# Kernel optimization log

Hardware: AMD Instinct MI355X
Metric: run time of the kernel (lower is better)

## Reference

```python
import jax, jax.numpy as jnp
from jax import lax
import numpy as np

B, C, H, W = 4, 1024, 64, 64
HEAD_DIM = 8
HEADS = C // HEAD_DIM  # 128
EPS = 1e-15
BN_EPS = 1e-5
DN = ('NCHW', 'OIHW', 'NCHW')


def setup_inputs() -> dict:
    key = jax.random.key(0)
    ks = jax.random.split(key, 8)
    s = lambda k, shp, scale: jax.random.normal(k, shp, jnp.float32) * scale
    return {
        'x': s(ks[0], (B, C, H, W), 1.0),
        'Wq': s(ks[1], (C, C), C ** -0.5),
        'Wk': s(ks[2], (C, C), C ** -0.5),
        'Wv': s(ks[3], (C, C), C ** -0.5),
        'dw_w': s(ks[4], (3 * C, 1, 5, 5), 0.2),          # depthwise, groups=3C
        'pw_w': s(ks[5], (3 * C, HEAD_DIM, 1, 1), 0.3),   # 1x1 grouped, groups=3*heads
        'Wout': s(ks[6], (C, 2 * C), (2 * C) ** -0.5),
        'gamma': jnp.ones((C,), jnp.float32),
        'beta': jnp.zeros((C,), jnp.float32),
    }


def _forward(x, Wq, Wk, Wv, dw_w, pw_w, Wout, gamma, beta):
    b, c, h, w = x.shape
    n = h * w
    hbhwc = jnp.moveaxis(x, 1, -1)                      # B H W C
    q = hbhwc @ Wq.T
    k = hbhwc @ Wk.T
    v = hbhwc @ Wv.T
    qkv = jnp.moveaxis(jnp.concatenate([q, k, v], -1), -1, 1)  # B 3C H W
    # multiscale branch: depthwise kxk then grouped 1x1
    ms = lax.conv_general_dilated(qkv, dw_w, (1, 1), 'SAME',
                                  feature_group_count=3 * c, dimension_numbers=DN)
    ms = lax.conv_general_dilated(ms, pw_w, (1, 1), 'VALID',
                                  feature_group_count=3 * HEADS, dimension_numbers=DN)
    hs = jnp.concatenate([qkv, ms], axis=1)             # B 6C H W
    hs = hs.astype(jnp.float32).reshape(b, -1, 3 * HEAD_DIM, n)  # B ht 3d N
    q, k, v = jnp.split(hs, 3, axis=2)                  # each B ht d N
    q = jax.nn.relu(q)
    k = jax.nn.relu(k)
    v = jnp.pad(v, ((0, 0), (0, 0), (0, 1), (0, 0)), constant_values=1.0)  # B ht d+1 N
    scores = jnp.einsum('bhdn,bhen->bhde', v, k)        # B ht d+1 d
    out = jnp.einsum('bhde,bhen->bhdn', scores, q)      # B ht d+1 N
    out = out[:, :, :-1] / (out[:, :, -1:] + EPS)       # B ht d N
    out = out.reshape(b, -1, h, w)                      # B 2C H W
    out = jnp.moveaxis(jnp.moveaxis(out, 1, -1) @ Wout.T, -1, 1)  # B C H W
    # batch norm (batch statistics, affine)
    mean = out.mean(axis=(0, 2, 3), keepdims=True)
    var = out.var(axis=(0, 2, 3), keepdims=True)
    gb = lambda p: p[None, :, None, None]
    return (out - mean) * lax.rsqrt(var + BN_EPS) * gb(gamma) + gb(beta)


def reference(x, Wq, Wk, Wv, dw_w, pw_w, Wout, gamma, beta):
    return _forward(x, Wq, Wk, Wv, dw_w, pw_w, Wout, gamma, beta)
```

## Files before the change

### kernel.cpp

```cpp
#include <hip/hip_runtime.h>


typedef short bf16x8 __attribute__((ext_vector_type(8)));
typedef float f32x4 __attribute__((ext_vector_type(4)));

__device__ __forceinline__ float bf2f(unsigned short u) {
  union { unsigned int i; float f; } w; w.i = ((unsigned int)u) << 16; return w.f;
}
__device__ __forceinline__ unsigned short f2bf(float f) {
  union { float f; unsigned int i; } w; w.f = f;
  return (unsigned short)((w.i + 0x7fffu + ((w.i >> 16) & 1u)) >> 16);
}

__device__ __forceinline__ void gload16(const void* g, void* l) {
  __builtin_amdgcn_global_load_lds(
      (const __attribute__((address_space(1))) void*)g,
      (__attribute__((address_space(3))) void*)l, 16, 0, 0);
}

static constexpr int BB = 4, CC = 1024, NN = 4096;
static constexpr int C3 = 3 * CC;
static constexpr int C2 = 2 * CC;
static constexpr int MROWS = BB * NN;

__global__ __launch_bounds__(256) void k_transpose_both(const float* __restrict__ x,
                                                        float* __restrict__ xTf,
                                                        unsigned short* __restrict__ xTb) {
  __shared__ float tile[32][33];
  const int c0 = blockIdx.y << 5, n0 = blockIdx.x << 5;
  const int tx = threadIdx.x & 31, ty = threadIdx.x >> 5;
#pragma unroll
  for (int i = 0; i < 32; i += 8)
    tile[ty + i][tx] = x[((size_t)(c0 + ty + i)) * NN + n0 + tx];
  __syncthreads();
#pragma unroll
  for (int i = 0; i < 32; i += 8) {
    const float v = tile[tx][ty + i];
    const size_t idx = ((size_t)(n0 + ty + i)) * CC + c0 + tx;
    xTf[idx] = v;
    xTb[idx] = f2bf(v);
  }
}

__global__ void k_cvt(const float* __restrict__ src, unsigned short* __restrict__ dst, int n4) {
  int i = blockIdx.x * 256 + threadIdx.x;
  if (i < n4) {
    float4 v = ((const float4*)src)[i];
    ushort4 o;
    o.x = f2bf(v.x); o.y = f2bf(v.y); o.z = f2bf(v.z); o.w = f2bf(v.w);
    ((ushort4*)dst)[i] = o;
  }
}

__global__ __launch_bounds__(256) void k_wpack(const float* __restrict__ Wq,
                                               const float* __restrict__ Wk,
                                               const float* __restrict__ Wv,
                                               float* __restrict__ Wpack) {
  const int j = blockIdx.x;
  const int c = 24 * (j >> 3) + (j & 7);
  const float* src = (c < CC) ? (Wq + (size_t)c * CC)
                   : (c < 2 * CC) ? (Wk + (size_t)(c - CC) * CC)
                   : (Wv + (size_t)(c - 2 * CC) * CC);
  const int t = threadIdx.x;
  ((float4*)(Wpack + (size_t)j * CC))[t] = ((const float4*)src)[t];
}

__global__ __launch_bounds__(256) void k_wkv(const float* __restrict__ Wq,
                                             const float* __restrict__ Wk,
                                             const float* __restrict__ Wv,
                                             unsigned short* __restrict__ Wkv) {
  const int jj = blockIdx.x;
  const int c = 24 * (jj >> 4) + 8 + (jj & 15);
  const float* src = (c < CC) ? (Wq + (size_t)c * CC)
                   : (c < 2 * CC) ? (Wk + (size_t)(c - CC) * CC)
                   : (Wv + (size_t)(c - 2 * CC) * CC);
  const int t = threadIdx.x;
  float4 v = ((const float4*)src)[t];
  ushort4 o;
  o.x = f2bf(v.x); o.y = f2bf(v.y); o.z = f2bf(v.z); o.w = f2bf(v.w);
  ((ushort4*)(Wkv + (size_t)jj * CC))[t] = o;
}

__global__ __launch_bounds__(256) void gemm_kv(const unsigned short* __restrict__ A,
                                               const unsigned short* __restrict__ Bmat,
                                               float* __restrict__ qkvT) {
  __shared__ __align__(16) unsigned short lA[128 * 32];
  __shared__ __align__(16) unsigned short lB[128 * 32];
  const int bx = blockIdx.x, by = blockIdx.y;
  const int tid = threadIdx.x, lane = tid & 63, wid = tid >> 6;
  const int wm = wid >> 1, wn = wid & 1;
  const int K = CC;

  const int srow = wid * 32 + (lane >> 2);
  const int skoff = (lane & 3) * 8;
  const unsigned short* Ag = A + (size_t)(bx * 128 + srow) * K + skoff;
  const unsigned short* Bg = Bmat + (size_t)(by * 128 + srow) * K + skoff;
  unsigned short* lAw = &lA[(wid * 32) * 32];
  unsigned short* lBw = &lB[(wid * 32) * 32];

  f32x4 acc[4][4] = {};

  for (int kt = 0; kt < K; kt += 32) {
    gload16(Ag + kt, lAw);
    gload16(Ag + kt + (size_t)16 * K, lAw + 16 * 32);
    gload16(Bg + kt, lBw);
    gload16(Bg + kt + (size_t)16 * K, lBw + 16 * 32);
    __syncthreads();

    const int fr = lane & 15, fkk = (lane >> 4) * 8;
    bf16x8 af[4], bfr[4];
#pragma unroll
    for (int i = 0; i < 4; ++i) {
      af[i]  = *reinterpret_cast<const bf16x8*>(&lA[(wm * 64 + i * 16 + fr) * 32 + fkk]);
      bfr[i] = *reinterpret_cast<const bf16x8*>(&lB[(wn * 64 + i * 16 + fr) * 32 + fkk]);
    }
#pragma unroll
    for (int i = 0; i < 4; ++i)
#pragma unroll
      for (int j = 0; j < 4; ++j)
        acc[i][j] = __builtin_amdgcn_mfma_f32_16x16x32_bf16(af[i], bfr[j], acc[i][j], 0, 0, 0);
    __syncthreads();
  }

  const int fr = lane & 15, fg = lane >> 4;
#pragma unroll
  for (int i = 0; i < 4; ++i) {
    const int row0 = bx * 128 + wm * 64 + i * 16 + fg * 4;
#pragma unroll
    for (int j = 0; j < 4; ++j) {
      const int jj = by * 128 + wn * 64 + j * 16 + fr;
      const int c = 24 * (jj >> 4) + 8 + (jj & 15);
#pragma unroll
      for (int r = 0; r < 4; ++r)
        qkvT[(size_t)(row0 + r) * C3 + c] = acc[i][j][r];
    }
  }
}

__global__ __launch_bounds__(256) void k_qnp3(const float* __restrict__ xTf,
                                              const float* __restrict__ Wpack,
                                              float* __restrict__ qkvT) {
  constexpr int PITCH = 132;
  __shared__ float lA[16 * PITCH];
  __shared__ float lB[16 * PITCH];
  const int bm = blockIdx.x * 128, bj = blockIdx.y * 128;
  const int t = threadIdx.x;
  const int srow = t >> 1, kb = (t & 1) * 8;
  const int tj = t & 15, tm = t >> 4;

  const float* gA = xTf + (size_t)(bm + srow) * CC + kb;
  const float* gB = Wpack + (size_t)(bj + srow) * CC + kb;

  float acc[8][8] = {};

  float4 pa0 = *(const float4*)(gA);
  float4 pa1 = *(const float4*)(gA + 4);
  float4 pb0 = *(const float4*)(gB);
  float4 pb1 = *(const float4*)(gB + 4);

  for (int kp = 0; kp < CC; kp += 16) {
    __syncthreads();
#pragma unroll
    for (int i = 0; i < 4; ++i) {
      lA[(kb + i) * PITCH + srow]     = pa0[i];
      lA[(kb + 4 + i) * PITCH + srow] = pa1[i];
      lB[(kb + i) * PITCH + srow]     = pb0[i];
      lB[(kb + 4 + i) * PITCH + srow] = pb1[i];
    }
    __syncthreads();
    if (kp + 16 < CC) {
      pa0 = *(const float4*)(gA + kp + 16);
      pa1 = *(const float4*)(gA + kp + 20);
      pb0 = *(const float4*)(gB + kp + 16);
      pb1 = *(const float4*)(gB + kp + 20);
    }
#pragma unroll
    for (int kk = 0; kk < 16; ++kk) {
      const float4 a0 = *(const float4*)&lA[kk * PITCH + tm * 8];
      const float4 a1 = *(const float4*)&lA[kk * PITCH + tm * 8 + 4];
      const float4 b0 = *(const float4*)&lB[kk * PITCH + tj * 8];
      const float4 b1 = *(const float4*)&lB[kk * PITCH + tj * 8 + 4];
      const float av[8] = {a0.x, a0.y, a0.z, a0.w, a1.x, a1.y, a1.z, a1.w};
      const float bv[8] = {b0.x, b0.y, b0.z, b0.w, b1.x, b1.y, b1.z, b1.w};
#pragma unroll
      for (int i = 0; i < 8; ++i)
#pragma unroll
        for (int j = 0; j < 8; ++j)
          acc[i][j] = fmaf(av[i], bv[j], acc[i][j]);
    }
  }

  const int head = (bj >> 3) + tj;
  const int cbase = 24 * head;
#pragma unroll
  for (int i = 0; i < 8; ++i) {
    const int m = bm + tm * 8 + i;
    float* d = &qkvT[(size_t)m * C3 + cbase];
    *(float4*)d = make_float4(acc[i][0], acc[i][1], acc[i][2], acc[i][3]);
    *(float4*)(d + 4) = make_float4(acc[i][4], acc[i][5], acc[i][6], acc[i][7]);
  }
}

__global__ __launch_bounds__(256) void gemm_bt(const unsigned short* __restrict__ A,
                                               const unsigned short* __restrict__ Bmat,
                                               float* __restrict__ Cout,
                                               int M, int N, int K) {
  __shared__ __align__(16) unsigned short lA[128 * 32];
  __shared__ __align__(16) unsigned short lB[128 * 32];
  const int bx = blockIdx.x, by = blockIdx.y;
  const int tid = threadIdx.x, lane = tid & 63, wid = tid >> 6;
  const int wm = wid >> 1, wn = wid & 1;

  const int srow = wid * 32 + (lane >> 2);
  const int skoff = (lane & 3) * 8;
  const unsigned short* Ag = A + (size_t)(bx * 128 + srow) * K + skoff;
  const unsigned short* Bg = Bmat + (size_t)(by * 128 + srow) * K + skoff;
  unsigned short* lAw = &lA[(wid * 32) * 32];
  unsigned short* lBw = &lB[(wid * 32) * 32];

  f32x4 acc[4][4] = {};

  for (int kt = 0; kt < K; kt += 32) {
    gload16(Ag + kt, lAw);
    gload16(Ag + kt + (size_t)16 * K, lAw + 16 * 32);
    gload16(Bg + kt, lBw);
    gload16(Bg + kt + (size_t)16 * K, lBw + 16 * 32);
    __syncthreads();

    const int fr = lane & 15, fkk = (lane >> 4) * 8;
    bf16x8 af[4], bfr[4];
#pragma unroll
    for (int i = 0; i < 4; ++i) {
      af[i]  = *reinterpret_cast<const bf16x8*>(&lA[(wm * 64 + i * 16 + fr) * 32 + fkk]);
      bfr[i] = *reinterpret_cast<const bf16x8*>(&lB[(wn * 64 + i * 16 + fr) * 32 + fkk]);
    }
#pragma unroll
    for (int i = 0; i < 4; ++i)
#pragma unroll
      for (int j = 0; j < 4; ++j)
        acc[i][j] = __builtin_amdgcn_mfma_f32_16x16x32_bf16(af[i], bfr[j], acc[i][j], 0, 0, 0);
    __syncthreads();
  }

  const int fr = lane & 15, fg = lane >> 4;
#pragma unroll
  for (int i = 0; i < 4; ++i) {
    const int row0 = bx * 128 + wm * 64 + i * 16 + fg * 4;
#pragma unroll
    for (int j = 0; j < 4; ++j) {
      const int col = by * 128 + wn * 64 + j * 16 + fr;
#pragma unroll
      for (int r = 0; r < 4; ++r)
        Cout[(size_t)(row0 + r) * N + col] = acc[i][j][r];
    }
  }
}

__global__ __launch_bounds__(256) void k_conv_ms(const float* __restrict__ qkvT,
                                                 const float* __restrict__ dw_w,
                                                 const float* __restrict__ pw_w,
                                                 float* __restrict__ msT) {
  __shared__ __align__(16) float tin[20][20][8];
  __shared__ float wdw[8][25];
  __shared__ float wpw[8][8];
  const int g = blockIdx.y;
  const int ty0 = (blockIdx.x >> 2) << 4, tx0 = (blockIdx.x & 3) << 4;
  const int tid = threadIdx.x;

  if (tid < 200) wdw[tid / 25][tid % 25] = dw_w[(size_t)(g * 8 + tid / 25) * 25 + tid % 25];
  if (tid < 64) wpw[tid >> 3][tid & 7] = pw_w[(size_t)(g * 8 + (tid >> 3)) * 8 + (tid & 7)];

  for (int p = tid; p < 400; p += 256) {
    const int iy = p / 20, ix = p % 20;
    const int gy = ty0 + iy - 2, gx = tx0 + ix - 2;
    float4 a = make_float4(0, 0, 0, 0), b4 = a;
    if (gy >= 0 && gy < 64 && gx >= 0 && gx < 64) {
      const float* s = &qkvT[((size_t)(gy * 64 + gx)) * C3 + g * 8];
      a = *(const float4*)s;
      b4 = *(const float4*)(s + 4);
    }
    *(float4*)&tin[iy][ix][0] = a;
    *(float4*)&tin[iy][ix][4] = b4;
  }
  __syncthreads();

  const int ty = tid >> 4, tx = tid & 15;
  double acc[8] = {0, 0, 0, 0, 0, 0, 0, 0};
#pragma unroll
  for (int dy = 0; dy < 5; ++dy)
#pragma unroll
    for (int dx = 0; dx < 5; ++dx) {
#pragma unroll
      for (int ci = 0; ci < 8; ++ci)
        acc[ci] += (double)wdw[ci][dy * 5 + dx] * (double)tin[ty + dy][tx + dx][ci];
    }
  float o[8];
#pragma unroll
  for (int co = 0; co < 8; ++co) {
    double s = 0.0;
#pragma unroll
    for (int ci = 0; ci < 8; ++ci) s += (double)wpw[co][ci] * acc[ci];
    o[co] = (float)s;
  }
  const int n = (ty0 + ty) * 64 + tx0 + tx;
  float* d = &msT[((size_t)n) * C3 + g * 8];
  *(float4*)d = make_float4(o[0], o[1], o[2], o[3]);
  *(float4*)(d + 4) = make_float4(o[4], o[5], o[6], o[7]);
}

__global__ __launch_bounds__(256) void k_attn(const float* __restrict__ qkvT,
                                              const float* __restrict__ msT,
                                              unsigned short* __restrict__ attn) {
  const int h = blockIdx.x;
  const float* src = (h < 128) ? qkvT + h * 24 : msT + (h - 128) * 24;
  const int tid = threadIdx.x, lane = tid & 63, wid = tid >> 6;

  float s[72];
#pragma unroll
  for (int i = 0; i < 72; ++i) s[i] = 0.f;

  for (int n = tid; n < NN; n += 256) {
    const float* p = src + (size_t)n * C3;
    float4 k0 = *(const float4*)(p + 8), k1 = *(const float4*)(p + 12);
    float4 v0 = *(const float4*)(p + 16), v1 = *(const float4*)(p + 20);
    float kf[8] = {fmaxf(k0.x, 0.f), fmaxf(k0.y, 0.f), fmaxf(k0.z, 0.f), fmaxf(k0.w, 0.f),
                   fmaxf(k1.x, 0.f), fmaxf(k1.y, 0.f), fmaxf(k1.z, 0.f), fmaxf(k1.w, 0.f)};
    float vf[8] = {v0.x, v0.y, v0.z, v0.w, v1.x, v1.y, v1.z, v1.w};
#pragma unroll
    for (int d = 0; d < 8; ++d)
#pragma unroll
      for (int e = 0; e < 8; ++e) s[d * 8 + e] += vf[d] * kf[e];
#pragma unroll
    for (int e = 0; e < 8; ++e) s[64 + e] += kf[e];
  }

  __shared__ float red[4][72];
  __shared__ float sc[72];
#pragma unroll
  for (int i = 0; i < 72; ++i) {
    float v = s[i];
#pragma unroll
    for (int off = 32; off > 0; off >>= 1) v += __shfl_xor(v, off, 64);
    if (lane == 0) red[wid][i] = v;
  }
  __syncthreads();
  if (tid < 72) sc[tid] = red[0][tid] + red[1][tid] + red[2][tid] + red[3][tid];
  __syncthreads();

  float sl[72];
#pragma unroll
  for (int i = 0; i < 72; ++i) sl[i] = sc[i];

  for (int n = tid; n < NN; n += 256) {
    const float* p = src + (size_t)n * C3;
    float4 q0 = *(const float4*)p, q1 = *(const float4*)(p + 4);
    float qf[8] = {fmaxf(q0.x, 0.f), fmaxf(q0.y, 0.f), fmaxf(q0.z, 0.f), fmaxf(q0.w, 0.f),
                   fmaxf(q1.x, 0.f), fmaxf(q1.y, 0.f), fmaxf(q1.z, 0.f), fmaxf(q1.w, 0.f)};
    float o[9];
#pragma unroll
    for (int d = 0; d < 9; ++d) {
      float t = 0.f;
#pragma unroll
      for (int e = 0; e < 8; ++e) t += sl[d * 8 + e] * qf[e];
      o[d] = t;
    }
    const float inv = 1.f / (o[8] + 1e-15f);
    union { unsigned short u[8]; uint4 v; } res;
#pragma unroll
    for (int d = 0; d < 8; ++d) res.u[d] = f2bf(o[d] * inv);
    *(uint4*)&attn[((size_t)n) * C2 + h * 8] = res.v;
  }
}

__global__ __launch_bounds__(256) void k_bn_stats(const float* __restrict__ out2,
                                                  float* __restrict__ part) {
  const int ch = blockIdx.x * 256 + threadIdx.x;
  const int r0 = blockIdx.y << 8;
  float s = 0.f, s2 = 0.f;
  for (int i = 0; i < 256; ++i) {
    float v = out2[(size_t)(r0 + i) * CC + ch];
    s += v; s2 += v * v;
  }
  part[((size_t)blockIdx.y * 2 + 0) * CC + ch] = s;
  part[((size_t)blockIdx.y * 2 + 1) * CC + ch] = s2;
}

__global__ __launch_bounds__(256) void k_bn_reduce(const float* __restrict__ part,
                                                   float* __restrict__ stats) {
  const int ch = blockIdx.x * 256 + threadIdx.x;
  float s = 0.f, s2 = 0.f;
  for (int i = 0; i < 64; ++i) {
    s += part[((size_t)i * 2 + 0) * CC + ch];
    s2 += part[((size_t)i * 2 + 1) * CC + ch];
  }
  stats[ch] = s;
  stats[CC + ch] = s2;
}

__global__ __launch_bounds__(256) void k_bn_apply(const float* __restrict__ out2,
                                                  const float* __restrict__ stats,
                                                  const float* __restrict__ gamma,
                                                  const float* __restrict__ beta,
                                                  float* __restrict__ out) {
  __shared__ float tile[32][33];
  const int b = blockIdx.z;
  const int c0 = blockIdx.y << 5, n0 = blockIdx.x << 5;
  const int tx = threadIdx.x & 31, ty = threadIdx.x >> 5;
  const int c = c0 + tx;
  const float mean = stats[c] * (1.f / 16384.f);
  const float var = stats[CC + c] * (1.f / 16384.f) - mean * mean;
  const float scale = gamma[c] * rsqrtf(var + 1e-5f);
  const float shift = beta[c] - mean * scale;
#pragma unroll
  for (int i = 0; i < 32; i += 8)
    tile[ty + i][tx] = out2[((size_t)b * NN + n0 + ty + i) * CC + c] * scale + shift;
  __syncthreads();
#pragma unroll
  for (int i = 0; i < 32; i += 8)
    out[((size_t)b * CC + c0 + ty + i) * NN + n0 + tx] = tile[tx][ty + i];
}

extern "C" void kernel_launch(void* const* d_in, const int* in_sizes, int n_in,
                              void* d_out, int out_size, void* d_ws, size_t ws_size,
                              hipStream_t stream) {
  const float* x     = (const float*)d_in[0];
  const float* Wq    = (const float*)d_in[1];
  const float* Wk    = (const float*)d_in[2];
  const float* Wv    = (const float*)d_in[3];
  const float* dw_w  = (const float*)d_in[4];
  const float* pw_w  = (const float*)d_in[5];
  const float* Wout  = (const float*)d_in[6];
  const float* gamma = (const float*)d_in[7];
  const float* beta  = (const float*)d_in[8];
  float* out = (float*)d_out;
  (void)ws_size; (void)in_sizes; (void)n_in; (void)out_size;

  char* ws = (char*)d_ws;
  const size_t MB = 1024 * 1024;
  float*          qkvT = (float*)(ws + 0);
  float*          msT  = (float*)(ws + 48 * MB);
  float*          xTf  = (float*)(ws + 96 * MB);
  unsigned short* xTb  = (unsigned short*)(ws + 112 * MB);
  unsigned short* Wkv  = (unsigned short*)(ws + 120 * MB);
  float*          Wpack= (float*)(ws + 126 * MB);
  unsigned short* WoutB= (unsigned short*)(ws + 130 * MB);
  float*          part = (float*)(ws + 134 * MB);
  float*          stats= (float*)(ws + 135 * MB);
  float*          out2 = (float*)(ws + 0);
  unsigned short* attnB= (unsigned short*)d_out;

  k_wkv<<<dim3(C2), 256, 0, stream>>>(Wq, Wk, Wv, Wkv);
  k_wpack<<<dim3(CC), 256, 0, stream>>>(Wq, Wk, Wv, Wpack);
  k_cvt<<<dim3(CC * C2 / 4 / 256), 256, 0, stream>>>(Wout, WoutB, CC * C2 / 4);

  for (int b = 0; b < BB; ++b) {
    k_transpose_both<<<dim3(NN / 32, CC / 32), 256, 0, stream>>>(x + (size_t)b * CC * NN, xTf, xTb);
    gemm_kv<<<dim3(NN / 128, C2 / 128), 256, 0, stream>>>(xTb, Wkv, qkvT);
    k_qnp3<<<dim3(NN / 128, CC / 128), 256, 0, stream>>>(xTf, Wpack, qkvT);
    k_conv_ms<<<dim3(16, C3 / 8), 256, 0, stream>>>(qkvT, dw_w, pw_w, msT);
    k_attn<<<dim3(256), 256, 0, stream>>>(qkvT, msT, attnB + (size_t)b * NN * C2);
  }

  gemm_bt<<<dim3(MROWS / 128, CC / 128), 256, 0, stream>>>(attnB, WoutB, out2, MROWS, CC, C2);

  k_bn_stats<<<dim3(CC / 256, 64), 256, 0, stream>>>(out2, part);
  k_bn_reduce<<<dim3(CC / 256), 256, 0, stream>>>(part, stats);
  k_bn_apply<<<dim3(NN / 32, CC / 32, BB), 256, 0, stream>>>(out2, stats, gamma, beta, out);
}
```

Measured before the change: 1.382 ms.

## Batch Q projection across all images with wider FP32 tiles, split Q/KV buffers

The input transpose and the FP32 query projection are hoisted out of the per-batch loop. The projection now runs as one GEMM over all 16K rows with a 128x256 tile and 8x16 outputs per thread, for more register reuse and fewer launches. Q and KV are stored in separate dense buffers instead of one interleaved qkvT layout, and the conv and attention kernels read them through per-stream strides. The output GEMM grid is also swapped so that blocks sharing an A row-tile run adjacently. In exchange the workspace grows, some buffers are aliased, and register pressure in the projection kernel rises.

Result: faster. 1.297 ms (-6.1%).

```diff
diff --git a/kernel.cpp b/kernel.cpp
--- a/kernel.cpp
+++ b/kernel.cpp
@@ -27,16 +27,17 @@
                                                         float* __restrict__ xTf,
                                                         unsigned short* __restrict__ xTb) {
   __shared__ float tile[32][33];
+  const int b = blockIdx.z;
   const int c0 = blockIdx.y << 5, n0 = blockIdx.x << 5;
   const int tx = threadIdx.x & 31, ty = threadIdx.x >> 5;
 #pragma unroll
   for (int i = 0; i < 32; i += 8)
-    tile[ty + i][tx] = x[((size_t)(c0 + ty + i)) * NN + n0 + tx];
+    tile[ty + i][tx] = x[((size_t)b * CC + c0 + ty + i) * NN + n0 + tx];
   __syncthreads();
 #pragma unroll
   for (int i = 0; i < 32; i += 8) {
     const float v = tile[tx][ty + i];
-    const size_t idx = ((size_t)(n0 + ty + i)) * CC + c0 + tx;
+    const size_t idx = ((size_t)b * NN + n0 + ty + i) * CC + c0 + tx;
     xTf[idx] = v;
     xTb[idx] = f2bf(v);
   }
@@ -83,7 +84,7 @@
 
 __global__ __launch_bounds__(256) void gemm_kv(const unsigned short* __restrict__ A,
                                                const unsigned short* __restrict__ Bmat,
-                                               float* __restrict__ qkvT) {
+                                               float* __restrict__ kvT) {
   __shared__ __align__(16) unsigned short lA[128 * 32];
   __shared__ __align__(16) unsigned short lB[128 * 32];
   const int bx = blockIdx.x, by = blockIdx.y;
@@ -129,43 +130,51 @@
 #pragma unroll
     for (int j = 0; j < 4; ++j) {
       const int jj = by * 128 + wn * 64 + j * 16 + fr;
-      const int c = 24 * (jj >> 4) + 8 + (jj & 15);
 #pragma unroll
       for (int r = 0; r < 4; ++r)
-        qkvT[(size_t)(row0 + r) * C3 + c] = acc[i][j][r];
-    }
-  }
-}
-
-__global__ __launch_bounds__(256) void k_qnp3(const float* __restrict__ xTf,
+        kvT[(size_t)(row0 + r) * C2 + jj] = acc[i][j][r];
+    }
+  }
+}
+
+__global__ __launch_bounds__(256) void k_qnp6(const float* __restrict__ xTf,
                                               const float* __restrict__ Wpack,
-                                              float* __restrict__ qkvT) {
-  constexpr int PITCH = 132;
-  __shared__ float lA[16 * PITCH];
-  __shared__ float lB[16 * PITCH];
-  const int bm = blockIdx.x * 128, bj = blockIdx.y * 128;
+                                              float* __restrict__ qAll) {
+  __shared__ float lA[16 * 132];
+  __shared__ float lB[16 * 320];
+  const int bj = blockIdx.x * 256;
+  const int bm = blockIdx.y * 128;
   const int t = threadIdx.x;
-  const int srow = t >> 1, kb = (t & 1) * 8;
-  const int tj = t & 15, tm = t >> 4;
-
-  const float* gA = xTf + (size_t)(bm + srow) * CC + kb;
-  const float* gB = Wpack + (size_t)(bj + srow) * CC + kb;
-
-  float acc[8][8] = {};
-
-  float4 pa0 = *(const float4*)(gA);
+  const int tm = t >> 4, tj = t & 15;
+  const int arow = t >> 1, akh = (t & 1) * 8;
+  const int bcol = t + ((t >> 4) << 2);
+
+  const float* gA = xTf + (size_t)(bm + arow) * CC + akh;
+  const float* gB = Wpack + (size_t)(bj + t) * CC;
+
+  float acc[8][16];
+#pragma unroll
+  for (int i = 0; i < 8; ++i)
+#pragma unroll
+    for (int j = 0; j < 16; ++j) acc[i][j] = 0.f;
+
+  float4 pa0 = *(const float4*)gA;
   float4 pa1 = *(const float4*)(gA + 4);
-  float4 pb0 = *(const float4*)(gB);
+  float4 pb0 = *(const float4*)gB;
   float4 pb1 = *(const float4*)(gB + 4);
+  float4 pb2 = *(const float4*)(gB + 8);
+  float4 pb3 = *(const float4*)(gB + 12);
 
   for (int kp = 0; kp < CC; kp += 16) {
     __syncthreads();
 #pragma unroll
     for (int i = 0; i < 4; ++i) {
-      lA[(kb + i) * PITCH + srow]     = pa0[i];
-      lA[(kb + 4 + i) * PITCH + srow] = pa1[i];
-      lB[(kb + i) * PITCH + srow]     = pb0[i];
-      lB[(kb + 4 + i) * PITCH + srow] = pb1[i];
+      lA[(akh + i) * 132 + arow]     = pa0[i];
+      lA[(akh + 4 + i) * 132 + arow] = pa1[i];
+      lB[(i) * 320 + bcol]      = pb0[i];
+      lB[(4 + i) * 320 + bcol]  = pb1[i];
+      lB[(8 + i) * 320 + bcol]  = pb2[i];
+      lB[(12 + i) * 320 + bcol] = pb3[i];
     }
     __syncthreads();
     if (kp + 16 < CC) {
@@ -173,31 +182,35 @@
       pa1 = *(const float4*)(gA + kp + 20);
       pb0 = *(const float4*)(gB + kp + 16);
       pb1 = *(const float4*)(gB + kp + 20);
+      pb2 = *(const float4*)(gB + kp + 24);
+      pb3 = *(const float4*)(gB + kp + 28);
     }
 #pragma unroll
     for (int kk = 0; kk < 16; ++kk) {
-      const float4 a0 = *(const float4*)&lA[kk * PITCH + tm * 8];
-      const float4 a1 = *(const float4*)&lA[kk * PITCH + tm * 8 + 4];
-      const float4 b0 = *(const float4*)&lB[kk * PITCH + tj * 8];
-      const float4 b1 = *(const float4*)&lB[kk * PITCH + tj * 8 + 4];
-      const float av[8] = {a0.x, a0.y, a0.z, a0.w, a1.x, a1.y, a1.z, a1.w};
-      const float bv[8] = {b0.x, b0.y, b0.z, b0.w, b1.x, b1.y, b1.z, b1.w};
+      const float4 a0 = *(const float4*)&lA[kk * 132 + tm * 8];
+      const float4 a1 = *(const float4*)&lA[kk * 132 + tm * 8 + 4];
+      const float4 b0 = *(const float4*)&lB[kk * 320 + tj * 20];
+      const float4 b1 = *(const float4*)&lB[kk * 320 + tj * 20 + 4];
+      const float4 b2 = *(const float4*)&lB[kk * 320 + tj * 20 + 8];
+      const float4 b3 = *(const float4*)&lB[kk * 320 + tj * 20 + 12];
+      const float av[8]  = {a0.x, a0.y, a0.z, a0.w, a1.x, a1.y, a1.z, a1.w};
+      const float bv[16] = {b0.x, b0.y, b0.z, b0.w, b1.x, b1.y, b1.z, b1.w,
+                            b2.x, b2.y, b2.z, b2.w, b3.x, b3.y, b3.z, b3.w};
 #pragma unroll
       for (int i = 0; i < 8; ++i)
 #pragma unroll
-        for (int j = 0; j < 8; ++j)
+        for (int j = 0; j < 16; ++j)
           acc[i][j] = fmaf(av[i], bv[j], acc[i][j]);
     }
   }
 
-  const int head = (bj >> 3) + tj;
-  const int cbase = 24 * head;
 #pragma unroll
   for (int i = 0; i < 8; ++i) {
-    const int m = bm + tm * 8 + i;
-    float* d = &qkvT[(size_t)m * C3 + cbase];
-    *(float4*)d = make_float4(acc[i][0], acc[i][1], acc[i][2], acc[i][3]);
-    *(float4*)(d + 4) = make_float4(acc[i][4], acc[i][5], acc[i][6], acc[i][7]);
+    float* row = qAll + (size_t)(bm + tm * 8 + i) * CC + bj + tj * 16;
+    *(float4*)(row)      = make_float4(acc[i][0],  acc[i][1],  acc[i][2],  acc[i][3]);
+    *(float4*)(row + 4)  = make_float4(acc[i][4],  acc[i][5],  acc[i][6],  acc[i][7]);
+    *(float4*)(row + 8)  = make_float4(acc[i][8],  acc[i][9],  acc[i][10], acc[i][11]);
+    *(float4*)(row + 12) = make_float4(acc[i][12], acc[i][13], acc[i][14], acc[i][15]);
   }
 }
 
@@ -207,7 +220,7 @@
                                                int M, int N, int K) {
   __shared__ __align__(16) unsigned short lA[128 * 32];
   __shared__ __align__(16) unsigned short lB[128 * 32];
-  const int bx = blockIdx.x, by = blockIdx.y;
+  const int bx = blockIdx.y, by = blockIdx.x;
   const int tid = threadIdx.x, lane = tid & 63, wid = tid >> 6;
   const int wm = wid >> 1, wn = wid & 1;
 
@@ -256,7 +269,8 @@
   }
 }
 
-__global__ __launch_bounds__(256) void k_conv_ms(const float* __restrict__ qkvT,
+__global__ __launch_bounds__(256) void k_conv_ms(const float* __restrict__ qAll,
+                                                 const float* __restrict__ kvT,
                                                  const float* __restrict__ dw_w,
                                                  const float* __restrict__ pw_w,
                                                  float* __restrict__ msT) {
@@ -267,6 +281,13 @@
   const int ty0 = (blockIdx.x >> 2) << 4, tx0 = (blockIdx.x & 3) << 4;
   const int tid = threadIdx.x;
 
+  const int tg = g / 3, r = g % 3;
+  const float* src;
+  int stride;
+  if (r == 0)      { src = qAll + tg * 8;        stride = CC; }
+  else if (r == 1) { src = kvT + tg * 16;        stride = C2; }
+  else             { src = kvT + tg * 16 + 8;    stride = C2; }
+
   if (tid < 200) wdw[tid / 25][tid % 25] = dw_w[(size_t)(g * 8 + tid / 25) * 25 + tid % 25];
   if (tid < 64) wpw[tid >> 3][tid & 7] = pw_w[(size_t)(g * 8 + (tid >> 3)) * 8 + (tid & 7)];
 
@@ -275,7 +296,7 @@
     const int gy = ty0 + iy - 2, gx = tx0 + ix - 2;
     float4 a = make_float4(0, 0, 0, 0), b4 = a;
     if (gy >= 0 && gy < 64 && gx >= 0 && gx < 64) {
-      const float* s = &qkvT[((size_t)(gy * 64 + gx)) * C3 + g * 8];
+      const float* s = src + (size_t)(gy * 64 + gx) * stride;
       a = *(const float4*)s;
       b4 = *(const float4*)(s + 4);
     }
@@ -308,11 +329,23 @@
   *(float4*)(d + 4) = make_float4(o[4], o[5], o[6], o[7]);
 }
 
-__global__ __launch_bounds__(256) void k_attn(const float* __restrict__ qkvT,
+__global__ __launch_bounds__(256) void k_attn(const float* __restrict__ qAll,
+                                              const float* __restrict__ kvT,
                                               const float* __restrict__ msT,
                                               unsigned short* __restrict__ attn) {
   const int h = blockIdx.x;
-  const float* src = (h < 128) ? qkvT + h * 24 : msT + (h - 128) * 24;
+  const float *pq, *pk, *pv;
+  int sq, sk, sv;
+  if (h < 128) {
+    pq = qAll + h * 8;  sq = CC;
+    pk = kvT + h * 16;  sk = C2;
+    pv = pk + 8;        sv = C2;
+  } else {
+    const float* m0 = msT + (size_t)(h - 128) * 24;
+    pq = m0;      sq = C3;
+    pk = m0 + 8;  sk = C3;
+    pv = m0 + 16; sv = C3;
+  }
   const int tid = threadIdx.x, lane = tid & 63, wid = tid >> 6;
 
   float s[72];
@@ -320,9 +353,10 @@
   for (int i = 0; i < 72; ++i) s[i] = 0.f;
 
   for (int n = tid; n < NN; n += 256) {
-    const float* p = src + (size_t)n * C3;
-    float4 k0 = *(const float4*)(p + 8), k1 = *(const float4*)(p + 12);
-    float4 v0 = *(const float4*)(p + 16), v1 = *(const float4*)(p + 20);
+    float4 k0 = *(const float4*)(pk + (size_t)n * sk);
+    float4 k1 = *(const float4*)(pk + (size_t)n * sk + 4);
+    float4 v0 = *(const float4*)(pv + (size_t)n * sv);
+    float4 v1 = *(const float4*)(pv + (size_t)n * sv + 4);
     float kf[8] = {fmaxf(k0.x, 0.f), fmaxf(k0.y, 0.f), fmaxf(k0.z, 0.f), fmaxf(k0.w, 0.f),
                    fmaxf(k1.x, 0.f), fmaxf(k1.y, 0.f), fmaxf(k1.z, 0.f), fmaxf(k1.w, 0.f)};
     float vf[8] = {v0.x, v0.y, v0.z, v0.w, v1.x, v1.y, v1.z, v1.w};
@@ -352,8 +386,8 @@
   for (int i = 0; i < 72; ++i) sl[i] = sc[i];
 
   for (int n = tid; n < NN; n += 256) {
-    const float* p = src + (size_t)n * C3;
-    float4 q0 = *(const float4*)p, q1 = *(const float4*)(p + 4);
+    float4 q0 = *(const float4*)(pq + (size_t)n * sq);
+    float4 q1 = *(const float4*)(pq + (size_t)n * sq + 4);
     float qf[8] = {fmaxf(q0.x, 0.f), fmaxf(q0.y, 0.f), fmaxf(q0.z, 0.f), fmaxf(q0.w, 0.f),
                    fmaxf(q1.x, 0.f), fmaxf(q1.y, 0.f), fmaxf(q1.z, 0.f), fmaxf(q1.w, 0.f)};
     float o[9];
@@ -437,15 +471,16 @@
 
   char* ws = (char*)d_ws;
   const size_t MB = 1024 * 1024;
-  float*          qkvT = (float*)(ws + 0);
-  float*          msT  = (float*)(ws + 48 * MB);
-  float*          xTf  = (float*)(ws + 96 * MB);
-  unsigned short* xTb  = (unsigned short*)(ws + 112 * MB);
-  unsigned short* Wkv  = (unsigned short*)(ws + 120 * MB);
-  float*          Wpack= (float*)(ws + 126 * MB);
-  unsigned short* WoutB= (unsigned short*)(ws + 130 * MB);
-  float*          part = (float*)(ws + 134 * MB);
-  float*          stats= (float*)(ws + 135 * MB);
+  float*          qAll = (float*)(ws + 0);
+  float*          xTf  = (float*)(ws + 64 * MB);
+  float*          msT  = (float*)(ws + 64 * MB);
+  float*          kvT  = (float*)(ws + 112 * MB);
+  unsigned short* xTb  = (unsigned short*)(ws + 144 * MB);
+  unsigned short* Wkv  = (unsigned short*)(ws + 176 * MB);
+  float*          Wpack= (float*)(ws + 180 * MB);
+  unsigned short* WoutB= (unsigned short*)(ws + 184 * MB);
+  float*          part = (float*)(ws + 188 * MB);
+  float*          stats= (float*)(ws + 189 * MB);
   float*          out2 = (float*)(ws + 0);
   unsigned short* attnB= (unsigned short*)d_out;
 
@@ -453,15 +488,19 @@
   k_wpack<<<dim3(CC), 256, 0, stream>>>(Wq, Wk, Wv, Wpack);
   k_cvt<<<dim3(CC * C2 / 4 / 256), 256, 0, stream>>>(Wout, WoutB, CC * C2 / 4);
 
+  k_transpose_both<<<dim3(NN / 32, CC / 32, BB), 256, 0, stream>>>(x, xTf, xTb);
+
+  k_qnp6<<<dim3(CC / 256, MROWS / 128), 256, 0, stream>>>(xTf, Wpack, qAll);
+
   for (int b = 0; b < BB; ++b) {
-    k_transpose_both<<<dim3(NN / 32, CC / 32), 256, 0, stream>>>(x + (size_t)b * CC * NN, xTf, xTb);
-    gemm_kv<<<dim3(NN / 128, C2 / 128), 256, 0, stream>>>(xTb, Wkv, qkvT);
-    k_qnp3<<<dim3(NN / 128, CC / 128), 256, 0, stream>>>(xTf, Wpack, qkvT);
-    k_conv_ms<<<dim3(16, C3 / 8), 256, 0, stream>>>(qkvT, dw_w, pw_w, msT);
-    k_attn<<<dim3(256), 256, 0, stream>>>(qkvT, msT, attnB + (size_t)b * NN * C2);
-  }
-
-  gemm_bt<<<dim3(MROWS / 128, CC / 128), 256, 0, stream>>>(attnB, WoutB, out2, MROWS, CC, C2);
+    const float* qAll_b = qAll + (size_t)b * NN * CC;
+    gemm_kv<<<dim3(NN / 128, C2 / 128), 256, 0, stream>>>(
+        xTb + (size_t)b * NN * CC, Wkv, kvT);
+    k_conv_ms<<<dim3(16, C3 / 8), 256, 0, stream>>>(qAll_b, kvT, dw_w, pw_w, msT);
+    k_attn<<<dim3(256), 256, 0, stream>>>(qAll_b, kvT, msT, attnB + (size_t)b * NN * C2);
+  }
+
+  gemm_bt<<<dim3(CC / 128, MROWS / 128), 256, 0, stream>>>(attnB, WoutB, out2, MROWS, CC, C2);
 
   k_bn_stats<<<dim3(CC / 256, 64), 256, 0, stream>>>(out2, part);
   k_bn_reduce<<<dim3(CC / 256), 256, 0, stream>>>(part, stats);
```
